# Kernel optimization log

Hardware: AMD Instinct MI355X
Metric: run time of the kernel (lower is better)

Reference implementation:

```python
import jax, jax.numpy as jnp
import numpy as np

HIDDEN_DIM = 640
VOCAB_SIZE = 1024


def setup_inputs() -> dict:
    key = jax.random.key(0)
    kf, kp, kw, kb = jax.random.split(key, 4)
    B, T, U, H, V = 8, 256, 64, HIDDEN_DIM, VOCAB_SIZE
    f = jax.random.normal(kf, (B, T, H), dtype=jnp.float32)
    p = jax.random.normal(kp, (B, U, H), dtype=jnp.float32)
    # nn.Linear default init: U(-1/sqrt(H), 1/sqrt(H))
    bound = 1.0 / np.sqrt(H)
    W = jax.random.uniform(kw, (V, H), minval=-bound, maxval=bound, dtype=jnp.float32)
    b = jax.random.uniform(kb, (V,), minval=-bound, maxval=bound, dtype=jnp.float32)
    return {"f": f, "p": p, "W": W, "b": b}


def reference(f, p, W, b):
    # f: (B,T,H), p: (B,U,H) -> combined: (B,T,U,H)
    combined = f[:, :, None, :] + p[:, None, :, :]
    h = jax.nn.relu(combined)
    # Linear: h @ W^T + b -> (B,T,U,V)
    logits = jnp.einsum('btuh,vh->btuv', h, W) + b
    return logits
```

## Files before the change

### kernel.cpp

```cpp
#include <hip/hip_runtime.h>
#include <hip/hip_bf16.h>

#define BDIM 8
#define TDIM 256
#define UDIM 64
#define HDIM 640
#define VDIM 1024

typedef __attribute__((ext_vector_type(8))) short short8;
typedef __attribute__((ext_vector_type(4))) float f32x4;

__device__ __forceinline__ ushort f2bf(float x) {
    union { float f; unsigned int u; } v; v.f = x;
    unsigned int r = (v.u + 0x7fffu + ((v.u >> 16) & 1u)) >> 16;
    return (ushort)r;
}

__global__ void cvt_w_kernel(const float* __restrict__ W, ushort* __restrict__ Wb) {
    int i = (blockIdx.x * 256 + threadIdx.x) * 4;
    f32x4 w = *(const f32x4*)(W + i);
    ushort4 o;
    o.x = f2bf(w[0]); o.y = f2bf(w[1]); o.z = f2bf(w[2]); o.w = f2bf(w[3]);
    *(ushort4*)(Wb + i) = o;
}

template <bool USE_WB>
__global__ __launch_bounds__(256) void joint_gemm_kernel(
    const float* __restrict__ f,
    const float* __restrict__ p,
    const float* __restrict__ Wf,
    const ushort* __restrict__ Wb,
    const float* __restrict__ bias,
    float* __restrict__ out)
{
    __shared__ ushort Alds[128 * 64];
    __shared__ ushort Blds[128 * 64];

    const int tid  = threadIdx.x;
    const int lane = tid & 63;
    const int wave = tid >> 6;
    const int wm   = wave >> 1;
    const int wn   = wave & 1;

    const int bid   = blockIdx.x;
    const int work  = (bid & 7) * 1024 + (bid >> 3);
    const int mtile = work >> 3;
    const int ntile = work & 7;
    const int m0 = mtile * 128;
    const int v0 = ntile * 128;

    const int b  = m0 >> 14;
    const int t0 = (m0 >> 6) & (TDIM - 1);

    const float*  fbase = f + (size_t)(b * TDIM + t0) * HDIM;
    const float*  pbase = p + (size_t)b * UDIM * HDIM;
    const ushort* wbbase = Wb + (size_t)v0 * HDIM;
    const float*  wfbase = Wf + (size_t)v0 * HDIM;

    f32x4 acc[4][4];
    #pragma unroll
    for (int i = 0; i < 4; ++i)
        #pragma unroll
        for (int j = 0; j < 4; ++j)
            acc[i][j] = (f32x4)0.0f;

    for (int kt = 0; kt < HDIM / 64; ++kt) {
        const int k0 = kt * 64;
        __syncthreads();

        if (USE_WB) {
            #pragma unroll
            for (int it = 0; it < 4; ++it) {
                const int c   = it * 256 + tid;
                const int row = c >> 3;
                const int j   = c & 7;
                const ushort* src = wbbase + row * HDIM + k0 + ((j ^ (row & 7)) << 3);
                __builtin_amdgcn_global_load_lds(
                    (const __attribute__((address_space(1))) void*)src,
                    (__attribute__((address_space(3))) void*)(&Blds[(it * 256 + wave * 64) * 8]),
                    16, 0, 0);
            }
        } else {
            #pragma unroll
            for (int it = 0; it < 4; ++it) {
                const int c   = it * 256 + tid;
                const int row = c >> 3;
                const int j   = c & 7;
                const float* wp = wfbase + row * HDIM + k0 + j * 8;
                f32x4 w0 = *(const f32x4*)wp;
                f32x4 w1 = *(const f32x4*)(wp + 4);
                short8 wv;
                #pragma unroll
                for (int e = 0; e < 4; ++e) {
                    wv[e]     = (short)f2bf(w0[e]);
                    wv[e + 4] = (short)f2bf(w1[e]);
                }
                *(short8*)(&Blds[(row * 8 + (j ^ (row & 7))) * 8]) = wv;
            }
        }

        #pragma unroll
        for (int it = 0; it < 4; ++it) {
            const int c   = it * 256 + tid;
            const int row = c >> 3;
            const int j   = c & 7;
            const float* fp_ = fbase + (row >> 6) * HDIM + k0 + j * 8;
            const float* pp_ = pbase + (row & 63) * HDIM + k0 + j * 8;
            f32x4 f0 = *(const f32x4*)fp_;
            f32x4 f1 = *(const f32x4*)(fp_ + 4);
            f32x4 p0 = *(const f32x4*)pp_;
            f32x4 p1 = *(const f32x4*)(pp_ + 4);
            short8 hv;
            #pragma unroll
            for (int e = 0; e < 4; ++e) {
                float a0 = f0[e] + p0[e]; a0 = fmaxf(a0, 0.0f);
                float a1 = f1[e] + p1[e]; a1 = fmaxf(a1, 0.0f);
                hv[e]     = (short)f2bf(a0);
                hv[e + 4] = (short)f2bf(a1);
            }
            *(short8*)(&Alds[(row * 8 + (j ^ (row & 7))) * 8]) = hv;
        }

        __syncthreads();

        #pragma unroll
        for (int ks = 0; ks < 2; ++ks) {
            short8 afr[4], bfr[4];
            #pragma unroll
            for (int mi = 0; mi < 4; ++mi) {
                const int r = wm * 64 + mi * 16 + (lane & 15);
                const int j = ks * 4 + (lane >> 4);
                afr[mi] = *(const short8*)(&Alds[(r * 8 + (j ^ (r & 7))) * 8]);
            }
            #pragma unroll
            for (int ni = 0; ni < 4; ++ni) {
                const int r = wn * 64 + ni * 16 + (lane & 15);
                const int j = ks * 4 + (lane >> 4);
                bfr[ni] = *(const short8*)(&Blds[(r * 8 + (j ^ (r & 7))) * 8]);
            }
            #pragma unroll
            for (int mi = 0; mi < 4; ++mi)
                #pragma unroll
                for (int ni = 0; ni < 4; ++ni)
                    acc[mi][ni] = __builtin_amdgcn_mfma_f32_16x16x32_bf16(
                        afr[mi], bfr[ni], acc[mi][ni], 0, 0, 0);
        }
    }

    #pragma unroll
    for (int ni = 0; ni < 4; ++ni) {
        const int col = v0 + wn * 64 + ni * 16 + (lane & 15);
        const float bv = bias[col];
        #pragma unroll
        for (int mi = 0; mi < 4; ++mi) {
            const int rbase = m0 + wm * 64 + mi * 16 + ((lane >> 4) << 2);
            #pragma unroll
            for (int reg = 0; reg < 4; ++reg) {
                out[(size_t)(rbase + reg) * VDIM + col] = acc[mi][ni][reg] + bv;
            }
        }
    }
}

extern "C" void kernel_launch(void* const* d_in, const int* in_sizes, int n_in,
                              void* d_out, int out_size, void* d_ws, size_t ws_size,
                              hipStream_t stream) {
    const float* f    = (const float*)d_in[0];
    const float* p    = (const float*)d_in[1];
    const float* W    = (const float*)d_in[2];
    const float* bias = (const float*)d_in[3];
    float* out = (float*)d_out;

    const int grid = (131072 / 128) * (VDIM / 128);

    const size_t wb_bytes = (size_t)VDIM * HDIM * sizeof(ushort);
    if (ws_size >= wb_bytes) {
        ushort* Wb = (ushort*)d_ws;
        cvt_w_kernel<<<640, 256, 0, stream>>>(W, Wb);
        joint_gemm_kernel<true><<<grid, 256, 0, stream>>>(f, p, W, Wb, bias, out);
    } else {
        joint_gemm_kernel<false><<<grid, 256, 0, stream>>>(f, p, W, nullptr, bias, out);
    }
}
```

Measured before the change: 370.6 us.

## Materialize bf16 joint activations in workspace, then run a pure bf16 GEMM

Adds a pre-pass kernel that computes relu(f+p) once per (b,t,u,h), converts it to bf16 and writes it to workspace. A separate GEMM kernel then loads both operands straight into LDS with async global_load_lds. This drops the eightfold per-N-tile recomputation and the fp32 global loads from the GEMM's A path. The cost is writing and re-reading a 131072x640 bf16 buffer (about 168 MB) plus an extra launch, and the path needs a larger workspace, falling back to the fused kernel otherwise.

```diff
diff --git a/kernel.cpp b/kernel.cpp
--- a/kernel.cpp
+++ b/kernel.cpp
@@ -6,6 +6,8 @@
 #define UDIM 64
 #define HDIM 640
 #define VDIM 1024
+
+#define MDIM (BDIM * TDIM * UDIM)
 
 typedef __attribute__((ext_vector_type(8))) short short8;
 typedef __attribute__((ext_vector_type(4))) float f32x4;
@@ -24,14 +26,143 @@
     *(ushort4*)(Wb + i) = o;
 }
 
-template <bool USE_WB>
-__global__ __launch_bounds__(256) void joint_gemm_kernel(
-    const float* __restrict__ f,
-    const float* __restrict__ p,
-    const float* __restrict__ Wf,
+__global__ __launch_bounds__(256) void build_h_kernel(
+    const float* __restrict__ f, const float* __restrict__ p,
+    ushort* __restrict__ h)
+{
+    const int tid = threadIdx.x;
+    const int row = (blockIdx.x << 5) + (tid >> 3);
+    const int j0  = tid & 7;
+    const int b = row >> 14;
+    const int t = (row >> 6) & (TDIM - 1);
+    const int u = row & (UDIM - 1);
+    const float* frow = f + (size_t)(b * TDIM + t) * HDIM;
+    const float* prow = p + (size_t)(b * UDIM + u) * HDIM;
+    ushort* hrow = h + (size_t)row * HDIM;
+    #pragma unroll
+    for (int it = 0; it < HDIM / 64; ++it) {
+        const int k = (j0 + it * 8) * 8;
+        f32x4 f0 = *(const f32x4*)(frow + k);
+        f32x4 f1 = *(const f32x4*)(frow + k + 4);
+        f32x4 p0 = *(const f32x4*)(prow + k);
+        f32x4 p1 = *(const f32x4*)(prow + k + 4);
+        short8 hv;
+        #pragma unroll
+        for (int e = 0; e < 4; ++e) {
+            float a0 = fmaxf(f0[e] + p0[e], 0.0f);
+            float a1 = fmaxf(f1[e] + p1[e], 0.0f);
+            hv[e]     = (short)f2bf(a0);
+            hv[e + 4] = (short)f2bf(a1);
+        }
+        *(short8*)(hrow + k) = hv;
+    }
+}
+
+__global__ __launch_bounds__(256) void hgemm_kernel(
+    const ushort* __restrict__ h,
     const ushort* __restrict__ Wb,
     const float* __restrict__ bias,
     float* __restrict__ out)
+{
+    __shared__ ushort Alds[128 * 64];
+    __shared__ ushort Blds[128 * 64];
+
+    const int tid  = threadIdx.x;
+    const int lane = tid & 63;
+    const int wave = tid >> 6;
+    const int wm   = wave >> 1;
+    const int wn   = wave & 1;
+
+    const int bid   = blockIdx.x;
+    const int work  = (bid & 7) * 1024 + (bid >> 3);
+    const int mtile = work >> 3;
+    const int ntile = work & 7;
+    const int m0 = mtile * 128;
+    const int v0 = ntile * 128;
+
+    const ushort* hbase  = h  + (size_t)m0 * HDIM;
+    const ushort* wbbase = Wb + (size_t)v0 * HDIM;
+
+    f32x4 acc[4][4];
+    #pragma unroll
+    for (int i = 0; i < 4; ++i)
+        #pragma unroll
+        for (int j = 0; j < 4; ++j)
+            acc[i][j] = (f32x4)0.0f;
+
+    for (int kt = 0; kt < HDIM / 64; ++kt) {
+        const int k0 = kt * 64;
+        __syncthreads();
+
+        #pragma unroll
+        for (int it = 0; it < 4; ++it) {
+            const int c   = it * 256 + tid;
+            const int row = c >> 3;
+            const int j   = c & 7;
+            const ushort* src = hbase + row * HDIM + k0 + ((j ^ (row & 7)) << 3);
+            __builtin_amdgcn_global_load_lds(
+                (const __attribute__((address_space(1))) void*)src,
+                (__attribute__((address_space(3))) void*)(&Alds[(it * 256 + wave * 64) * 8]),
+                16, 0, 0);
+        }
+        #pragma unroll
+        for (int it = 0; it < 4; ++it) {
+            const int c   = it * 256 + tid;
+            const int row = c >> 3;
+            const int j   = c & 7;
+            const ushort* src = wbbase + row * HDIM + k0 + ((j ^ (row & 7)) << 3);
+            __builtin_amdgcn_global_load_lds(
+                (const __attribute__((address_space(1))) void*)src,
+                (__attribute__((address_space(3))) void*)(&Blds[(it * 256 + wave * 64) * 8]),
+                16, 0, 0);
+        }
+
+        __syncthreads();
+
+        #pragma unroll
+        for (int ks = 0; ks < 2; ++ks) {
+            short8 afr[4], bfr[4];
+            #pragma unroll
+            for (int mi = 0; mi < 4; ++mi) {
+                const int r = wm * 64 + mi * 16 + (lane & 15);
+                const int j = ks * 4 + (lane >> 4);
+                afr[mi] = *(const short8*)(&Alds[(r * 8 + (j ^ (r & 7))) * 8]);
+            }
+            #pragma unroll
+            for (int ni = 0; ni < 4; ++ni) {
+                const int r = wn * 64 + ni * 16 + (lane & 15);
+                const int j = ks * 4 + (lane >> 4);
+                bfr[ni] = *(const short8*)(&Blds[(r * 8 + (j ^ (r & 7))) * 8]);
+            }
+            #pragma unroll
+            for (int mi = 0; mi < 4; ++mi)
+                #pragma unroll
+                for (int ni = 0; ni < 4; ++ni)
+                    acc[mi][ni] = __builtin_amdgcn_mfma_f32_16x16x32_bf16(
+                        afr[mi], bfr[ni], acc[mi][ni], 0, 0, 0);
+        }
+    }
+
+    #pragma unroll
+    for (int ni = 0; ni < 4; ++ni) {
+        const int col = v0 + wn * 64 + ni * 16 + (lane & 15);
+        const float bv = bias[col];
+        #pragma unroll
+        for (int mi = 0; mi < 4; ++mi) {
+            const int rbase = m0 + wm * 64 + mi * 16 + ((lane >> 4) << 2);
+            #pragma unroll
+            for (int reg = 0; reg < 4; ++reg) {
+                out[(size_t)(rbase + reg) * VDIM + col] = acc[mi][ni][reg] + bv;
+            }
+        }
+    }
+}
+
+template <bool USE_WB>
+__global__ __launch_bounds__(256) void joint_gemm_kernel(
+    const float* __restrict__ f, const float* __restrict__ p,
+    const float* __restrict__ Wf, const ushort* __restrict__ Wb,
+    const float* __restrict__ bias, float* __restrict__ out)
 {
     __shared__ ushort Alds[128 * 64];
     __shared__ ushort Blds[128 * 64];
@@ -113,8 +244,8 @@
             short8 hv;
             #pragma unroll
             for (int e = 0; e < 4; ++e) {
-                float a0 = f0[e] + p0[e]; a0 = fmaxf(a0, 0.0f);
-                float a1 = f1[e] + p1[e]; a1 = fmaxf(a1, 0.0f);
+                float a0 = fmaxf(f0[e] + p0[e], 0.0f);
+                float a1 = fmaxf(f1[e] + p1[e], 0.0f);
                 hv[e]     = (short)f2bf(a0);
                 hv[e + 4] = (short)f2bf(a1);
             }
@@ -171,12 +302,20 @@
     const float* bias = (const float*)d_in[3];
     float* out = (float*)d_out;
 
-    const int grid = (131072 / 128) * (VDIM / 128);
+    const int grid = (MDIM / 128) * (VDIM / 128);
 
     const size_t wb_bytes = (size_t)VDIM * HDIM * sizeof(ushort);
-    if (ws_size >= wb_bytes) {
+    const size_t h_bytes  = (size_t)MDIM * HDIM * sizeof(ushort);
+
+    if (ws_size >= wb_bytes + h_bytes) {
         ushort* Wb = (ushort*)d_ws;
-        cvt_w_kernel<<<640, 256, 0, stream>>>(W, Wb);
+        ushort* h  = (ushort*)((char*)d_ws + wb_bytes);
+        cvt_w_kernel<<<(VDIM * HDIM) / 1024, 256, 0, stream>>>(W, Wb);
+        build_h_kernel<<<MDIM / 32, 256, 0, stream>>>(f, p, h);
+        hgemm_kernel<<<grid, 256, 0, stream>>>(h, Wb, bias, out);
+    } else if (ws_size >= wb_bytes) {
+        ushort* Wb = (ushort*)d_ws;
+        cvt_w_kernel<<<(VDIM * HDIM) / 1024, 256, 0, stream>>>(W, Wb);
         joint_gemm_kernel<true><<<grid, 256, 0, stream>>>(f, p, W, Wb, bias, out);
     } else {
         joint_gemm_kernel<false><<<grid, 256, 0, stream>>>(f, p, W, nullptr, bias, out);
```

New measurement: 432.4 us. 1.17x slower.
